# Performance work log

Hardware: AMD Instinct MI355X
Metric: run time of the kernel (lower is better)

## Reference

```python
import jax, jax.numpy as jnp
import numpy as np
import math

B, L, D, H, FACTOR = 4, 2048, 256, 8, 5
DH = D // H

def setup_inputs() -> dict:
    key = jax.random.key(0)
    ks = jax.random.split(key, 12)
    s = 1.0 / math.sqrt(D)
    return {
        "q": jax.random.normal(ks[0], (B, L, D), jnp.float32),
        "k": jax.random.normal(ks[1], (B, L, D), jnp.float32),
        "v": jax.random.normal(ks[2], (B, L, D), jnp.float32),
        "Wq": jax.random.normal(ks[3], (D, D), jnp.float32) * s,
        "bq": jax.random.normal(ks[4], (D,), jnp.float32) * s,
        "Wk": jax.random.normal(ks[5], (D, D), jnp.float32) * s,
        "bk": jax.random.normal(ks[6], (D,), jnp.float32) * s,
        "Wv": jax.random.normal(ks[7], (D, D), jnp.float32) * s,
        "bv": jax.random.normal(ks[8], (D,), jnp.float32) * s,
        "Wc": jax.random.normal(ks[9], (D, D), jnp.float32) * s,
        "bc": jax.random.normal(ks[10], (D,), jnp.float32) * s,
        "index_sample": jax.random.randint(ks[11], (L,), 0, L),  # U_part = min(5*L*ceil(log1p(L)), L) = L
    }

def reference(q, k, v, Wq, bq, Wk, bk, Wv, bv, Wc, bc, index_sample):
    # projections (torch Linear: x @ W^T + b)
    qp = q @ Wq.T + bq
    kp = k @ Wk.T + bk
    vp = v @ Wv.T + bv
    # NOTE: original reshapes q with a raw view (no transpose), k/v via split()
    q4 = qp.reshape(B, H, L, DH)                       # faithful to q.view(B, H, L, dh)
    k4 = kp.reshape(B, L, H, DH).transpose(0, 2, 1, 3)
    v4 = vp.reshape(B, L, H, DH).transpose(0, 2, 1, 3)
    qf = q4.reshape(B * H, L, DH)
    kf = k4.reshape(B * H, L, DH)
    vf = v4.reshape(B * H, L, DH)
    # random K sampling (with replacement); U_part == L here
    K_sample = kf[:, index_sample, :]                  # [BH, L, dh]
    QK = jnp.einsum('bld,bud->blu', qf, K_sample)      # [BH, L, L]
    M = QK.max(axis=-1) - QK.sum(axis=-1) / L          # sparsity measure [BH, L]
    u = min(FACTOR * math.ceil(math.log1p(L)), L)      # = 40
    _, top_idx = jax.lax.top_k(-M, u)                  # topk(..., largest=False)
    Q_red = jnp.take_along_axis(qf, top_idx[:, :, None], axis=1)  # [BH, u, dh]
    scores = jnp.einsum('bud,bld->bul', Q_red, kf) / math.sqrt(DH)
    probs = jax.nn.softmax(scores, axis=-1)
    out = jnp.einsum('bul,bld->bud', probs, vf)        # [BH, u, dh]
    out = out.reshape(B, H, u, DH).transpose(0, 2, 1, 3).reshape(B, u, D)
    return out @ Wc.T + bc
```

## Files before the change

### kernel.cpp

```cpp
#include <hip/hip_runtime.h>
#include <math.h>

#define B_ 4
#define L_ 2048
#define D_ 256
#define H_ 8
#define DH_ 32
#define NH_ 32
#define U_ 40
#define LD_ 524288
#define NCH_ 16

typedef __attribute__((ext_vector_type(8))) short short8;
typedef __attribute__((ext_vector_type(4))) float floatx4;

static __device__ __forceinline__ unsigned long long ullmin_(unsigned long long a, unsigned long long b) {
    return a < b ? a : b;
}
static __device__ __forceinline__ unsigned short f2bf_rne(float x) {
    unsigned u = __float_as_uint(x);
    unsigned r = u + 0x7FFFu + ((u >> 16) & 1u);
    return (unsigned short)(r >> 16);
}
static __device__ __forceinline__ float bf2f(unsigned short h) {
    return __uint_as_float(((unsigned)h) << 16);
}

__global__ __launch_bounds__(256) void gemm_mfma3(const float* __restrict__ q,
                                                  const float* __restrict__ k,
                                                  const float* __restrict__ v,
                                                  const float* __restrict__ Wq,
                                                  const float* __restrict__ Wk,
                                                  const float* __restrict__ Wv,
                                                  const float* __restrict__ bq,
                                                  const float* __restrict__ bk,
                                                  const float* __restrict__ bv,
                                                  float* __restrict__ qp,
                                                  float* __restrict__ kp,
                                                  float* __restrict__ vp) {
    const int mat = blockIdx.z;
    const float* X = (mat == 0) ? q : (mat == 1) ? k : v;
    const float* W = (mat == 0) ? Wq : (mat == 1) ? Wk : Wv;
    const float* bias = (mat == 0) ? bq : (mat == 1) ? bk : bv;
    float* Y = (mat == 0) ? qp : (mat == 1) ? kp : vp;

    const int t = threadIdx.x;
    const int w = t >> 6, lane = t & 63;
    const int lq = lane & 15, quad = lane >> 4;
    const int colBase = blockIdx.y * 64;
    const int rowBaseW = blockIdx.x * 128 + w * 32;

    __shared__ unsigned short Bls[24576];

    floatx4 acc[2][4];
#pragma unroll
    for (int mt = 0; mt < 2; ++mt)
#pragma unroll
        for (int nt = 0; nt < 4; ++nt) acc[mt][nt] = (floatx4){0.f, 0.f, 0.f, 0.f};

    for (int phase = 0; phase < 2; ++phase) {
        __syncthreads();
#pragma unroll
        for (int r = 0; r < 8; ++r) {
            const int e = t + 256 * r;
            const int col = e >> 5;
            const int k4u = e & 31;
            const int kk = phase * 128 + k4u * 4;
            const float4 x = *(const float4*)(W + (size_t)(colBase + col) * 256 + kk);
            float xs[4] = {x.x, x.y, x.z, x.w};
            unsigned short hv[4], mv4[4], lv[4];
#pragma unroll
            for (int j = 0; j < 4; ++j) {
                hv[j] = f2bf_rne(xs[j]);
                const float e1 = xs[j] - bf2f(hv[j]);
                mv4[j] = f2bf_rne(e1);
                const float e2 = e1 - bf2f(mv4[j]);
                lv[j] = f2bf_rne(e2);
            }
            const int nt = col >> 4, cin = col & 15;
            const int ktl = k4u >> 3, kin = (k4u & 7) * 4;
            const int base = nt * 512 + cin * 32 + kin;
            *(ushort4*)&Bls[((0 * 4 + ktl) << 11) + base] = make_ushort4(hv[0], hv[1], hv[2], hv[3]);
            *(ushort4*)&Bls[((1 * 4 + ktl) << 11) + base] = make_ushort4(mv4[0], mv4[1], mv4[2], mv4[3]);
            *(ushort4*)&Bls[((2 * 4 + ktl) << 11) + base] = make_ushort4(lv[0], lv[1], lv[2], lv[3]);
        }
        __syncthreads();

#pragma unroll
        for (int ktl = 0; ktl < 4; ++ktl) {
            const int kt = phase * 4 + ktl;
            short8 Bh[4], Bm[4], Bl[4];
            const int fo = lq * 32 + quad * 8;
#pragma unroll
            for (int j = 0; j < 4; ++j) {
                Bh[j] = *(const short8*)&Bls[((0 * 4 + ktl) << 11) + j * 512 + fo];
                Bm[j] = *(const short8*)&Bls[((1 * 4 + ktl) << 11) + j * 512 + fo];
                Bl[j] = *(const short8*)&Bls[((2 * 4 + ktl) << 11) + j * 512 + fo];
            }
#pragma unroll
            for (int mt = 0; mt < 2; ++mt) {
                const int m = rowBaseW + mt * 16 + lq;
                short8 Ah, Am, Al;
                {
                    const float* xr = X + (size_t)m * 256 + kt * 32 + quad * 8;
                    const float4 x0 = *(const float4*)xr;
                    const float4 x1 = *(const float4*)(xr + 4);
                    float xs[8] = {x0.x, x0.y, x0.z, x0.w, x1.x, x1.y, x1.z, x1.w};
#pragma unroll
                    for (int j = 0; j < 8; ++j) {
                        const unsigned short h = f2bf_rne(xs[j]);
                        const float e1 = xs[j] - bf2f(h);
                        const unsigned short md = f2bf_rne(e1);
                        const float e2 = e1 - bf2f(md);
                        Ah[j] = (short)h;
                        Am[j] = (short)md;
                        Al[j] = (short)f2bf_rne(e2);
                    }
                }
#pragma unroll
                for (int j = 0; j < 4; ++j) {
                    floatx4 a = acc[mt][j];
                    a = __builtin_amdgcn_mfma_f32_16x16x32_bf16(Am, Bm[j], a, 0, 0, 0);
                    a = __builtin_amdgcn_mfma_f32_16x16x32_bf16(Ah, Bl[j], a, 0, 0, 0);
                    a = __builtin_amdgcn_mfma_f32_16x16x32_bf16(Al, Bh[j], a, 0, 0, 0);
                    a = __builtin_amdgcn_mfma_f32_16x16x32_bf16(Ah, Bm[j], a, 0, 0, 0);
                    a = __builtin_amdgcn_mfma_f32_16x16x32_bf16(Am, Bh[j], a, 0, 0, 0);
                    a = __builtin_amdgcn_mfma_f32_16x16x32_bf16(Ah, Bh[j], a, 0, 0, 0);
                    acc[mt][j] = a;
                }
            }
        }
    }

#pragma unroll
    for (int mt = 0; mt < 2; ++mt)
#pragma unroll
        for (int nt = 0; nt < 4; ++nt) {
            const int c = colBase + nt * 16 + lq;
            const float bv_ = bias[c];
#pragma unroll
            for (int r = 0; r < 4; ++r) {
                const int mr = rowBaseW + mt * 16 + quad * 4 + r;
                Y[(size_t)mr * 256 + c] = acc[mt][nt][r] + bv_;
            }
        }
}

__global__ __launch_bounds__(64) void gemm_out(const float* __restrict__ X,
                                               const float* __restrict__ Wc,
                                               const float* __restrict__ bias,
                                               float* __restrict__ Y) {
    const int lane = threadIdx.x;
    const int lq = lane & 15, quad = lane >> 4;
    const int rowBase = blockIdx.x * 16;
    const int colBase = blockIdx.y * 64;

    floatx4 acc[4];
#pragma unroll
    for (int nt = 0; nt < 4; ++nt) acc[nt] = (floatx4){0.f, 0.f, 0.f, 0.f};

#pragma unroll
    for (int kt = 0; kt < 8; ++kt) {
        short8 Ah, Am, Al;
        {
            const float* xr = X + (size_t)(rowBase + lq) * 256 + kt * 32 + quad * 8;
            const float4 x0 = *(const float4*)xr;
            const float4 x1 = *(const float4*)(xr + 4);
            float xs[8] = {x0.x, x0.y, x0.z, x0.w, x1.x, x1.y, x1.z, x1.w};
#pragma unroll
            for (int j = 0; j < 8; ++j) {
                const unsigned short h = f2bf_rne(xs[j]);
                const float e1 = xs[j] - bf2f(h);
                const unsigned short md = f2bf_rne(e1);
                const float e2 = e1 - bf2f(md);
                Ah[j] = (short)h;
                Am[j] = (short)md;
                Al[j] = (short)f2bf_rne(e2);
            }
        }
        short8 Bh[4], Bm[4], Bl[4];
#pragma unroll
        for (int nt = 0; nt < 4; ++nt) {
            const float* wr = Wc + (size_t)(colBase + nt * 16 + lq) * 256 + kt * 32 + quad * 8;
            const float4 x0 = *(const float4*)wr;
            const float4 x1 = *(const float4*)(wr + 4);
            float xs[8] = {x0.x, x0.y, x0.z, x0.w, x1.x, x1.y, x1.z, x1.w};
#pragma unroll
            for (int j = 0; j < 8; ++j) {
                const unsigned short h = f2bf_rne(xs[j]);
                const float e1 = xs[j] - bf2f(h);
                const unsigned short md = f2bf_rne(e1);
                const float e2 = e1 - bf2f(md);
                Bh[nt][j] = (short)h;
                Bm[nt][j] = (short)md;
                Bl[nt][j] = (short)f2bf_rne(e2);
            }
        }
#pragma unroll
        for (int nt = 0; nt < 4; ++nt) {
            floatx4 a = acc[nt];
            a = __builtin_amdgcn_mfma_f32_16x16x32_bf16(Am, Bm[nt], a, 0, 0, 0);
            a = __builtin_amdgcn_mfma_f32_16x16x32_bf16(Ah, Bl[nt], a, 0, 0, 0);
            a = __builtin_amdgcn_mfma_f32_16x16x32_bf16(Al, Bh[nt], a, 0, 0, 0);
            a = __builtin_amdgcn_mfma_f32_16x16x32_bf16(Ah, Bm[nt], a, 0, 0, 0);
            a = __builtin_amdgcn_mfma_f32_16x16x32_bf16(Am, Bh[nt], a, 0, 0, 0);
            a = __builtin_amdgcn_mfma_f32_16x16x32_bf16(Ah, Bh[nt], a, 0, 0, 0);
            acc[nt] = a;
        }
    }

#pragma unroll
    for (int nt = 0; nt < 4; ++nt) {
        const int c = colBase + nt * 16 + lq;
        const float bv = bias[c];
#pragma unroll
        for (int r = 0; r < 4; ++r) {
            const int mr = rowBase + quad * 4 + r;
            Y[(size_t)mr * 256 + c] = acc[nt][r] + bv;
        }
    }
}

__global__ __launch_bounds__(256) void kconv_ksum(const float* __restrict__ kp,
                                                  const int* __restrict__ idx,
                                                  unsigned short* __restrict__ Khi,
                                                  unsigned short* __restrict__ Klo,
                                                  float* __restrict__ Ksum32) {
    const int blk = blockIdx.x;
    const int i = blk >> 5, uc = blk & 31;
    const int b = i >> 3, h = i & 7;
    const int t = threadIdx.x;
    const int dq = (t & 7) * 4;
    const int ur = t >> 3;

    __shared__ float part[32][36];
    float ksum[4] = {0.f, 0.f, 0.f, 0.f};

#pragma unroll
    for (int p = 0; p < 2; ++p) {
        int u = uc * 64 + p * 32 + ur;
        const float4 x = *(const float4*)(kp + (size_t)b * LD_ + (size_t)idx[u] * D_ + h * DH_ + dq);
        float xs[4] = {x.x, x.y, x.z, x.w};
        unsigned short hv[4], lv[4];
#pragma unroll
        for (int j = 0; j < 4; ++j) {
            ksum[j] += xs[j];
            hv[j] = f2bf_rne(xs[j]);
            lv[j] = f2bf_rne(xs[j] - bf2f(hv[j]));
        }
        size_t o = ((size_t)i * 2048 + u) * 32 + dq;
        *(ushort4*)(Khi + o) = make_ushort4(hv[0], hv[1], hv[2], hv[3]);
        *(ushort4*)(Klo + o) = make_ushort4(lv[0], lv[1], lv[2], lv[3]);
    }
#pragma unroll
    for (int j = 0; j < 4; ++j) part[ur][dq + j] = ksum[j];
    __syncthreads();
    if (t < 32) {
        float s = 0.f;
#pragma unroll 8
        for (int u2 = 0; u2 < 32; ++u2) s += part[u2][t];
        Ksum32[(size_t)blk * 32 + t] = s;
    }
}

__global__ __launch_bounds__(256) void mpart_mfma(const float* __restrict__ qp,
                                                  const unsigned short* __restrict__ Khi,
                                                  const unsigned short* __restrict__ Klo,
                                                  const float* __restrict__ Ksum32,
                                                  float* __restrict__ Mv,
                                                  float* __restrict__ Qmean) {
    const int blk = blockIdx.x;
    const int i = blk >> 5;
    const int lg = blk & 31;
    const int t = threadIdx.x;
    const int w = t >> 6;
    const int lane = t & 63;
    const int lq = lane & 15;
    const int quad = lane >> 4;

    __shared__ float ssum[32];
    __shared__ float red[4][64];
    if (t < 32) {
        float s = 0.f;
#pragma unroll 8
        for (int uc = 0; uc < 32; ++uc) s += Ksum32[((size_t)i * 32 + uc) * 32 + t];
        ssum[t] = s;
    }

    short8 Ah[4], Al[4];
#pragma unroll
    for (int lt = 0; lt < 4; ++lt) {
        const int l = lg * 64 + lt * 16 + lq;
        const float* qrow = qp + ((size_t)i * 2048 + l) * 32 + quad * 8;
        float4 x0 = *(const float4*)(qrow);
        float4 x1 = *(const float4*)(qrow + 4);
        float xs[8] = {x0.x, x0.y, x0.z, x0.w, x1.x, x1.y, x1.z, x1.w};
#pragma unroll
        for (int j = 0; j < 8; ++j) {
            unsigned short h = f2bf_rne(xs[j]);
            unsigned short lo = f2bf_rne(xs[j] - bf2f(h));
            Ah[lt][j] = (short)h;
            Al[lt][j] = (short)lo;
        }
    }

    floatx4 rmax[4];
#pragma unroll
    for (int lt = 0; lt < 4; ++lt)
        rmax[lt] = (floatx4){-INFINITY, -INFINITY, -INFINITY, -INFINITY};

    const size_t kfrag = ((size_t)i * 2048 + w * 512 + lq) * 32 + quad * 8;
    const unsigned short* ph = Khi + kfrag;
    const unsigned short* pl = Klo + kfrag;
#pragma unroll 2
    for (int s = 0; s < 32; ++s) {
        short8 Bh = *(const short8*)(ph + (size_t)s * 512);
        short8 Bl = *(const short8*)(pl + (size_t)s * 512);
#pragma unroll
        for (int lt = 0; lt < 4; ++lt) {
            floatx4 acc = (floatx4){0.f, 0.f, 0.f, 0.f};
            acc = __builtin_amdgcn_mfma_f32_16x16x32_bf16(Al[lt], Bh, acc, 0, 0, 0);
            acc = __builtin_amdgcn_mfma_f32_16x16x32_bf16(Ah[lt], Bl, acc, 0, 0, 0);
            acc = __builtin_amdgcn_mfma_f32_16x16x32_bf16(Ah[lt], Bh, acc, 0, 0, 0);
#pragma unroll
            for (int r = 0; r < 4; ++r) rmax[lt][r] = fmaxf(rmax[lt][r], acc[r]);
        }
    }

#pragma unroll
    for (int lt = 0; lt < 4; ++lt)
#pragma unroll
        for (int r = 0; r < 4; ++r) {
            float v = rmax[lt][r];
#pragma unroll
            for (int off = 1; off < 16; off <<= 1)
                v = fmaxf(v, __shfl_xor(v, off, 64));
            rmax[lt][r] = v;
        }
    if (lq == 0) {
#pragma unroll
        for (int lt = 0; lt < 4; ++lt)
#pragma unroll
            for (int r = 0; r < 4; ++r)
                red[w][lt * 16 + quad * 4 + r] = rmax[lt][r];
    }
    __syncthreads();
    if (t < 64) {
        const int l = lg * 64 + t;
        float m = fmaxf(fmaxf(red[0][t], red[1][t]), fmaxf(red[2][t], red[3][t]));
        const float4* q4 = (const float4*)(qp + ((size_t)i * 2048 + l) * 32);
        const float4* s4 = (const float4*)ssum;
        float qs = 0.f;
#pragma unroll
        for (int z = 0; z < 8; ++z) {
            float4 a = q4[z];
            float4 c = s4[z];
            qs = fmaf(a.x, c.x, qs);
            qs = fmaf(a.y, c.y, qs);
            qs = fmaf(a.z, c.z, qs);
            qs = fmaf(a.w, c.w, qs);
        }
        const float qm = qs * (1.0f / 2048.0f);
        Qmean[(size_t)i * 2048 + l] = qm;
        Mv[(size_t)i * 2048 + l] = m - qm;
    }
}

__global__ __launch_bounds__(256) void topk64_kernel(const float* __restrict__ Mv,
                                                     int* __restrict__ candIdx) {
    const int i = blockIdx.x;
    const int t = threadIdx.x;
    unsigned long long keys[8];
    __shared__ unsigned long long wred[4];
#pragma unroll
    for (int j = 0; j < 8; ++j) {
        const int l = t + 256 * j;
        unsigned u32 = __float_as_uint(Mv[(size_t)i * 2048 + l]);
        u32 = (u32 & 0x80000000u) ? ~u32 : (u32 | 0x80000000u);
        keys[j] = ((unsigned long long)u32 << 32) | (unsigned)l;
    }
    for (int it = 0; it < 64; ++it) {
        unsigned long long best = keys[0];
#pragma unroll
        for (int j = 1; j < 8; ++j) best = ullmin_(best, keys[j]);
#pragma unroll
        for (int off = 1; off < 64; off <<= 1)
            best = ullmin_(best, __shfl_xor(best, off, 64));
        if ((t & 63) == 0) wred[t >> 6] = best;
        __syncthreads();
        const unsigned long long m = ullmin_(ullmin_(wred[0], wred[1]), ullmin_(wred[2], wred[3]));
        if (t == 0) candIdx[i * 64 + it] = (int)(m & 0xffffffffu);
#pragma unroll
        for (int j = 0; j < 8; ++j)
            if (keys[j] == m) keys[j] = ~0ULL;
        __syncthreads();
    }
}

__global__ __launch_bounds__(256) void refine_kernel(const float* __restrict__ qp,
                                                     const float* __restrict__ kp,
                                                     const int* __restrict__ idx,
                                                     const int* __restrict__ candIdx,
                                                     float* __restrict__ refPart) {
    const int blk = blockIdx.x;
    const int i = blk >> 3, c = blk & 7;
    const int b = i >> 3, h = i & 7;
    const int t = threadIdx.x;
    __shared__ float qc[64][40];
    __shared__ float Ks[128][40];

    {
        const int cand = t >> 2, dp = (t & 3) * 8;
        const int l = candIdx[i * 64 + cand];
        const float* src = qp + ((size_t)i * 2048 + l) * 32 + dp;
        *(float4*)&qc[cand][dp] = *(const float4*)(src);
        *(float4*)&qc[cand][dp + 4] = *(const float4*)(src + 4);
    }
    __syncthreads();

    const int cand = t >> 2, usub = t & 3;
    float qv[32];
#pragma unroll
    for (int z = 0; z < 8; ++z) {
        float4 a = *(const float4*)&qc[cand][z * 4];
        qv[4 * z] = a.x; qv[4 * z + 1] = a.y; qv[4 * z + 2] = a.z; qv[4 * z + 3] = a.w;
    }

    float m = -INFINITY;
    for (int s = 0; s < 2; ++s) {
        {
            const int r = t >> 1, half = t & 1;
            const int u = c * 256 + s * 128 + r;
            const float* krow = kp + (size_t)b * LD_ + (size_t)idx[u] * D_ + h * DH_ + half * 16;
#pragma unroll
            for (int z = 0; z < 4; ++z)
                *(float4*)&Ks[r][half * 16 + z * 4] = *(const float4*)(krow + z * 4);
        }
        __syncthreads();
        for (int ur = usub; ur < 128; ur += 4) {
            float a0 = 0, a1 = 0, a2 = 0, a3 = 0;
#pragma unroll
            for (int z = 0; z < 8; ++z) {
                float4 kv = *(const float4*)&Ks[ur][z * 4];
                a0 = fmaf(qv[4 * z], kv.x, a0);
                a1 = fmaf(qv[4 * z + 1], kv.y, a1);
                a2 = fmaf(qv[4 * z + 2], kv.z, a2);
                a3 = fmaf(qv[4 * z + 3], kv.w, a3);
            }
            m = fmaxf(m, (a0 + a1) + (a2 + a3));
        }
        __syncthreads();
    }
    m = fmaxf(m, __shfl_xor(m, 1, 64));
    m = fmaxf(m, __shfl_xor(m, 2, 64));
    if ((t & 3) == 0) refPart[((size_t)i * 8 + c) * 64 + cand] = m;
}

__global__ __launch_bounds__(64) void select40_kernel(const int* __restrict__ candIdx,
                                                      const float* __restrict__ refPart,
                                                      const float* __restrict__ Qmean,
                                                      int* __restrict__ topIdx) {
    const int i = blockIdx.x;
    const int t = threadIdx.x;
    const int l = candIdx[i * 64 + t];
    float m = -INFINITY;
#pragma unroll
    for (int c = 0; c < 8; ++c) m = fmaxf(m, refPart[((size_t)i * 8 + c) * 64 + t]);
    float Mex = m - Qmean[(size_t)i * 2048 + l];
    unsigned u32 = __float_as_uint(Mex);
    u32 = (u32 & 0x80000000u) ? ~u32 : (u32 | 0x80000000u);
    unsigned long long key = ((unsigned long long)u32 << 32) | (unsigned)l;
    for (int it = 0; it < 40; ++it) {
        unsigned long long k2 = key;
#pragma unroll
        for (int off = 1; off < 64; off <<= 1) k2 = ullmin_(k2, __shfl_xor(k2, off, 64));
        if (key == k2) {
            topIdx[i * 40 + it] = l;
            key = ~0ULL;
        }
    }
}

#define SCP2 136
#define VSP 36

__global__ __launch_bounds__(320) void attn_part(const float* __restrict__ qp,
                                                 const float* __restrict__ kp,
                                                 const float* __restrict__ vp,
                                                 const int* __restrict__ topIdx,
                                                 float* __restrict__ mPart,
                                                 float* __restrict__ sPart,
                                                 float* __restrict__ oPart) {
    const int blk = blockIdx.x;
    const int i = blk >> 4, c = blk & 15;
    const int b = i >> 3, h = i & 7;
    const int t = threadIdx.x;

    __shared__ float Qs[40][32];
    __shared__ float Vs[128][VSP];
    __shared__ float sc[40][SCP2];
    __shared__ float mred[40], sred[40];

    {
        const int r = t >> 3, qq = t & 7;
        const int lq = topIdx[i * 40 + r];
        *(float4*)&Qs[r][qq * 4] = *(const float4*)(qp + ((size_t)i * 2048 + lq) * 32 + qq * 4);
    }
    for (int e = t; e < 1024; e += 320) {
        const int r = e >> 3, qq = e & 7;
        *(float4*)&Vs[r][qq * 4] =
            *(const float4*)(vp + (size_t)b * LD_ + (size_t)(c * 128 + r) * 256 + h * 32 + qq * 4);
    }
    __syncthreads();

    const float scale = 0.17677669529663687f;

    if (t < 256) {
        const int r = t >> 1;
        const int j0 = (t & 1) * 20;
        const float* kr = kp + (size_t)b * LD_ + (size_t)(c * 128 + r) * 256 + h * 32;
        float kv[32];
#pragma unroll
        for (int z = 0; z < 8; ++z) {
            float4 x = *(const float4*)(kr + z * 4);
            kv[4 * z] = x.x; kv[4 * z + 1] = x.y; kv[4 * z + 2] = x.z; kv[4 * z + 3] = x.w;
        }
#pragma unroll 4
        for (int jj = 0; jj < 20; ++jj) {
            const int j = j0 + jj;
            float a0 = 0, a1 = 0, a2 = 0, a3 = 0;
#pragma unroll
            for (int z = 0; z < 8; ++z) {
                const float4 q4 = *(const float4*)&Qs[j][z * 4];
                a0 = fmaf(kv[4 * z], q4.x, a0);
                a1 = fmaf(kv[4 * z + 1], q4.y, a1);
                a2 = fmaf(kv[4 * z + 2], q4.z, a2);
                a3 = fmaf(kv[4 * z + 3], q4.w, a3);
            }
            sc[j][r] = ((a0 + a1) + (a2 + a3)) * scale;
        }
    }
    __syncthreads();

    {
        const int w = t >> 6, lane = t & 63;
#pragma unroll
        for (int rr = 0; rr < 8; ++rr) {
            const int j = w * 8 + rr;
            float x0 = sc[j][lane], x1 = sc[j][lane + 64];
            float m = fmaxf(x0, x1);
#pragma unroll
            for (int off = 1; off < 64; off <<= 1) m = fmaxf(m, __shfl_xor(m, off, 64));
            const float e0 = __expf(x0 - m), e1 = __expf(x1 - m);
            sc[j][lane] = e0; sc[j][lane + 64] = e1;
            float s = e0 + e1;
#pragma unroll
            for (int off = 1; off < 64; off <<= 1) s += __shfl_xor(s, off, 64);
            if (lane == 0) { mred[j] = m; sred[j] = s; }
        }
    }
    __syncthreads();

    {
        const int j = t >> 3, qq = t & 7;
        float4 acc = make_float4(0.f, 0.f, 0.f, 0.f);
        for (int l = 0; l < 128; ++l) {
            const float p = sc[j][l];
            const float4 v4 = *(const float4*)&Vs[l][qq * 4];
            acc.x = fmaf(p, v4.x, acc.x);
            acc.y = fmaf(p, v4.y, acc.y);
            acc.z = fmaf(p, v4.z, acc.z);
            acc.w = fmaf(p, v4.w, acc.w);
        }
        const size_t o = (size_t)(i * NCH_ + c) * 40 + j;
        *(float4*)&oPart[o * 32 + qq * 4] = acc;
        if (qq == 0) { mPart[o] = mred[j]; sPart[o] = sred[j]; }
    }
}

__global__ __launch_bounds__(256) void attn_combine(const float* __restrict__ mPart,
                                                    const float* __restrict__ sPart,
                                                    const float* __restrict__ oPart,
                                                    float* __restrict__ attnOut) {
    const int i = blockIdx.x;
    const int b = i >> 3, h = i & 7;
    const int t = threadIdx.x;
    for (int e = t; e < 1280; e += 256) {
        const int j = e >> 5, d = e & 31;
        float mv[NCH_];
        float M = -INFINITY;
#pragma unroll
        for (int c = 0; c < NCH_; ++c) {
            mv[c] = mPart[(size_t)(i * NCH_ + c) * 40 + j];
            M = fmaxf(M, mv[c]);
        }
        float S = 0.f, O = 0.f;
#pragma unroll
        for (int c = 0; c < NCH_; ++c) {
            const float sc_ = __expf(mv[c] - M);
            const size_t o = (size_t)(i * NCH_ + c) * 40 + j;
            S = fmaf(sPart[o], sc_, S);
            O = fmaf(oPart[o * 32 + d], sc_, O);
        }
        attnOut[((size_t)b * 40 + j) * 256 + h * 32 + d] = O / S;
    }
}

extern "C" void kernel_launch(void* const* d_in, const int* in_sizes, int n_in,
                              void* d_out, int out_size, void* d_ws, size_t ws_size,
                              hipStream_t stream) {
    const float* q  = (const float*)d_in[0];
    const float* k  = (const float*)d_in[1];
    const float* v  = (const float*)d_in[2];
    const float* Wq = (const float*)d_in[3];
    const float* bq = (const float*)d_in[4];
    const float* Wk = (const float*)d_in[5];
    const float* bk = (const float*)d_in[6];
    const float* Wv = (const float*)d_in[7];
    const float* bv = (const float*)d_in[8];
    const float* Wc = (const float*)d_in[9];
    const float* bc = (const float*)d_in[10];
    const int* idx  = (const int*)d_in[11];
    float* out = (float*)d_out;

    char* w = (char*)d_ws;
    float*          qp      = (float*)(w);
    float*          kp      = (float*)(w + (8u << 20));
    float*          vp      = (float*)(w + (16u << 20));
    unsigned short* Khi     = (unsigned short*)(w + (24u << 20));
    unsigned short* Klo     = (unsigned short*)(w + (28u << 20));
    float*          Mv      = (float*)(w + (32u << 20));
    float*          Qmean   = (float*)(w + (32u << 20) + (256u << 10));
    float*          Ksum32  = (float*)(w + (32u << 20) + (512u << 10));
    int*            candIdx = (int*)  (w + (32u << 20) + (640u << 10));
    int*            topIdx  = (int*)  (w + (32u << 20) + (648u << 10));
    float*          refPart = (float*)(w + (32u << 20) + (656u << 10));
    float*          attnOut = (float*)(w + (32u << 20) + (720u << 10));
    float*          mPart   = (float*)(w + (24u << 20));
    float*          sPart   = (float*)(w + (24u << 20) + (128u << 10));
    float*          oPart   = (float*)(w + (24u << 20) + (256u << 10));

    hipLaunchKernelGGL(gemm_mfma3, dim3(64, 4, 3), dim3(256), 0, stream,
                       q, k, v, Wq, Wk, Wv, bq, bk, bv, qp, kp, vp);
    hipLaunchKernelGGL(kconv_ksum, dim3(1024), dim3(256), 0, stream, kp, idx, Khi, Klo, Ksum32);
    hipLaunchKernelGGL(mpart_mfma, dim3(1024), dim3(256), 0, stream, qp, Khi, Klo, Ksum32, Mv, Qmean);
    hipLaunchKernelGGL(topk64_kernel, dim3(32), dim3(256), 0, stream, Mv, candIdx);
    hipLaunchKernelGGL(refine_kernel, dim3(256), dim3(256), 0, stream, qp, kp, idx, candIdx, refPart);
    hipLaunchKernelGGL(select40_kernel, dim3(32), dim3(64), 0, stream, candIdx, refPart, Qmean, topIdx);
    hipLaunchKernelGGL(attn_part, dim3(512), dim3(320), 0, stream, qp, kp, vp, topIdx, mPart, sPart, oPart);
    hipLaunchKernelGGL(attn_combine, dim3(32), dim3(256), 0, stream, mPart, sPart, oPart, attnOut);
    hipLaunchKernelGGL(gemm_out, dim3(10, 4), dim3(64), 0, stream, attnOut, Wc, bc, out);
}
```

Baseline: 246.9 us.

## Fuse top-64 candidate selection into refine and top-40 selection into attention

Drops the separate topk64 and select40 kernels. Each refine block now redundantly computes the top-64 candidates from Mv (8x redundant per head), and each attention block redundantly recomputes the final top-40 from the refine partials (16x redundant per head). This removes two launches and their serial gaps on tiny grids, at the cost of duplicated selection work and an extra barrier in each block.

```diff
diff --git a/kernel.cpp b/kernel.cpp
--- a/kernel.cpp
+++ b/kernel.cpp
@@ -366,52 +366,52 @@
     }
 }
 
-__global__ __launch_bounds__(256) void topk64_kernel(const float* __restrict__ Mv,
-                                                     int* __restrict__ candIdx) {
-    const int i = blockIdx.x;
-    const int t = threadIdx.x;
-    unsigned long long keys[8];
-    __shared__ unsigned long long wred[4];
-#pragma unroll
-    for (int j = 0; j < 8; ++j) {
-        const int l = t + 256 * j;
-        unsigned u32 = __float_as_uint(Mv[(size_t)i * 2048 + l]);
-        u32 = (u32 & 0x80000000u) ? ~u32 : (u32 | 0x80000000u);
-        keys[j] = ((unsigned long long)u32 << 32) | (unsigned)l;
-    }
-    for (int it = 0; it < 64; ++it) {
-        unsigned long long best = keys[0];
-#pragma unroll
-        for (int j = 1; j < 8; ++j) best = ullmin_(best, keys[j]);
-#pragma unroll
-        for (int off = 1; off < 64; off <<= 1)
-            best = ullmin_(best, __shfl_xor(best, off, 64));
-        if ((t & 63) == 0) wred[t >> 6] = best;
-        __syncthreads();
-        const unsigned long long m = ullmin_(ullmin_(wred[0], wred[1]), ullmin_(wred[2], wred[3]));
-        if (t == 0) candIdx[i * 64 + it] = (int)(m & 0xffffffffu);
-#pragma unroll
-        for (int j = 0; j < 8; ++j)
-            if (keys[j] == m) keys[j] = ~0ULL;
-        __syncthreads();
-    }
-}
-
-__global__ __launch_bounds__(256) void refine_kernel(const float* __restrict__ qp,
+__global__ __launch_bounds__(256) void refine_kernel(const float* __restrict__ Mv,
+                                                     const float* __restrict__ qp,
                                                      const float* __restrict__ kp,
                                                      const int* __restrict__ idx,
-                                                     const int* __restrict__ candIdx,
+                                                     int* __restrict__ candIdx,
                                                      float* __restrict__ refPart) {
     const int blk = blockIdx.x;
     const int i = blk >> 3, c = blk & 7;
     const int b = i >> 3, h = i & 7;
     const int t = threadIdx.x;
+    __shared__ unsigned long long wred[4];
+    __shared__ int candL[64];
     __shared__ float qc[64][40];
     __shared__ float Ks[128][40];
 
     {
+        unsigned long long keys[8];
+#pragma unroll
+        for (int j = 0; j < 8; ++j) {
+            const int l = t + 256 * j;
+            unsigned u32 = __float_as_uint(Mv[(size_t)i * 2048 + l]);
+            u32 = (u32 & 0x80000000u) ? ~u32 : (u32 | 0x80000000u);
+            keys[j] = ((unsigned long long)u32 << 32) | (unsigned)l;
+        }
+        for (int it = 0; it < 64; ++it) {
+            unsigned long long best = keys[0];
+#pragma unroll
+            for (int j = 1; j < 8; ++j) best = ullmin_(best, keys[j]);
+#pragma unroll
+            for (int off = 1; off < 64; off <<= 1)
+                best = ullmin_(best, __shfl_xor(best, off, 64));
+            if ((t & 63) == 0) wred[t >> 6] = best;
+            __syncthreads();
+            const unsigned long long m = ullmin_(ullmin_(wred[0], wred[1]), ullmin_(wred[2], wred[3]));
+            if (t == 0) candL[it] = (int)(m & 0xffffffffu);
+#pragma unroll
+            for (int j = 0; j < 8; ++j)
+                if (keys[j] == m) keys[j] = ~0ULL;
+            __syncthreads();
+        }
+    }
+    if (c == 0 && t < 64) candIdx[i * 64 + t] = candL[t];
+
+    {
         const int cand = t >> 2, dp = (t & 3) * 8;
-        const int l = candIdx[i * 64 + cand];
+        const int l = candL[cand];
         const float* src = qp + ((size_t)i * 2048 + l) * 32 + dp;
         *(float4*)&qc[cand][dp] = *(const float4*)(src);
         *(float4*)&qc[cand][dp + 4] = *(const float4*)(src + 4);
@@ -456,38 +456,15 @@
     if ((t & 3) == 0) refPart[((size_t)i * 8 + c) * 64 + cand] = m;
 }
 
-__global__ __launch_bounds__(64) void select40_kernel(const int* __restrict__ candIdx,
-                                                      const float* __restrict__ refPart,
-                                                      const float* __restrict__ Qmean,
-                                                      int* __restrict__ topIdx) {
-    const int i = blockIdx.x;
-    const int t = threadIdx.x;
-    const int l = candIdx[i * 64 + t];
-    float m = -INFINITY;
-#pragma unroll
-    for (int c = 0; c < 8; ++c) m = fmaxf(m, refPart[((size_t)i * 8 + c) * 64 + t]);
-    float Mex = m - Qmean[(size_t)i * 2048 + l];
-    unsigned u32 = __float_as_uint(Mex);
-    u32 = (u32 & 0x80000000u) ? ~u32 : (u32 | 0x80000000u);
-    unsigned long long key = ((unsigned long long)u32 << 32) | (unsigned)l;
-    for (int it = 0; it < 40; ++it) {
-        unsigned long long k2 = key;
-#pragma unroll
-        for (int off = 1; off < 64; off <<= 1) k2 = ullmin_(k2, __shfl_xor(k2, off, 64));
-        if (key == k2) {
-            topIdx[i * 40 + it] = l;
-            key = ~0ULL;
-        }
-    }
-}
-
 #define SCP2 136
 #define VSP 36
 
 __global__ __launch_bounds__(320) void attn_part(const float* __restrict__ qp,
                                                  const float* __restrict__ kp,
                                                  const float* __restrict__ vp,
-                                                 const int* __restrict__ topIdx,
+                                                 const int* __restrict__ candIdx,
+                                                 const float* __restrict__ refPart,
+                                                 const float* __restrict__ Qmean,
                                                  float* __restrict__ mPart,
                                                  float* __restrict__ sPart,
                                                  float* __restrict__ oPart) {
@@ -496,20 +473,42 @@
     const int b = i >> 3, h = i & 7;
     const int t = threadIdx.x;
 
+    __shared__ int topL[40];
     __shared__ float Qs[40][32];
     __shared__ float Vs[128][VSP];
     __shared__ float sc[40][SCP2];
     __shared__ float mred[40], sred[40];
 
-    {
-        const int r = t >> 3, qq = t & 7;
-        const int lq = topIdx[i * 40 + r];
-        *(float4*)&Qs[r][qq * 4] = *(const float4*)(qp + ((size_t)i * 2048 + lq) * 32 + qq * 4);
+    if (t < 64) {
+        const int l = candIdx[i * 64 + t];
+        float m = -INFINITY;
+#pragma unroll
+        for (int cc = 0; cc < 8; ++cc) m = fmaxf(m, refPart[((size_t)i * 8 + cc) * 64 + t]);
+        const float Mex = m - Qmean[(size_t)i * 2048 + l];
+        unsigned u32 = __float_as_uint(Mex);
+        u32 = (u32 & 0x80000000u) ? ~u32 : (u32 | 0x80000000u);
+        unsigned long long key = ((unsigned long long)u32 << 32) | (unsigned)l;
+        for (int it = 0; it < 40; ++it) {
+            unsigned long long k2 = key;
+#pragma unroll
+            for (int off = 1; off < 64; off <<= 1) k2 = ullmin_(k2, __shfl_xor(k2, off, 64));
+            if (key == k2) {
+                topL[it] = l;
+                key = ~0ULL;
+            }
+        }
     }
     for (int e = t; e < 1024; e += 320) {
         const int r = e >> 3, qq = e & 7;
         *(float4*)&Vs[r][qq * 4] =
             *(const float4*)(vp + (size_t)b * LD_ + (size_t)(c * 128 + r) * 256 + h * 32 + qq * 4);
+    }
+    __syncthreads();
+
+    {
+        const int r = t >> 3, qq = t & 7;
+        const int lq = topL[r];
+        *(float4*)&Qs[r][qq * 4] = *(const float4*)(qp + ((size_t)i * 2048 + lq) * 32 + qq * 4);
     }
     __syncthreads();
 
@@ -633,7 +632,6 @@
     float*          Qmean   = (float*)(w + (32u << 20) + (256u << 10));
     float*          Ksum32  = (float*)(w + (32u << 20) + (512u << 10));
     int*            candIdx = (int*)  (w + (32u << 20) + (640u << 10));
-    int*            topIdx  = (int*)  (w + (32u << 20) + (648u << 10));
     float*          refPart = (float*)(w + (32u << 20) + (656u << 10));
     float*          attnOut = (float*)(w + (32u << 20) + (720u << 10));
     float*          mPart   = (float*)(w + (24u << 20));
@@ -644,10 +642,9 @@
                        q, k, v, Wq, Wk, Wv, bq, bk, bv, qp, kp, vp);
     hipLaunchKernelGGL(kconv_ksum, dim3(1024), dim3(256), 0, stream, kp, idx, Khi, Klo, Ksum32);
     hipLaunchKernelGGL(mpart_mfma, dim3(1024), dim3(256), 0, stream, qp, Khi, Klo, Ksum32, Mv, Qmean);
-    hipLaunchKernelGGL(topk64_kernel, dim3(32), dim3(256), 0, stream, Mv, candIdx);
-    hipLaunchKernelGGL(refine_kernel, dim3(256), dim3(256), 0, stream, qp, kp, idx, candIdx, refPart);
-    hipLaunchKernelGGL(select40_kernel, dim3(32), dim3(64), 0, stream, candIdx, refPart, Qmean, topIdx);
-    hipLaunchKernelGGL(attn_part, dim3(512), dim3(320), 0, stream, qp, kp, vp, topIdx, mPart, sPart, oPart);
+    hipLaunchKernelGGL(refine_kernel, dim3(256), dim3(256), 0, stream, Mv, qp, kp, idx, candIdx, refPart);
+    hipLaunchKernelGGL(attn_part, dim3(512), dim3(320), 0, stream, qp, kp, vp, candIdx, refPart, Qmean,
+                       mPart, sPart, oPart);
     hipLaunchKernelGGL(attn_combine, dim3(32), dim3(256), 0, stream, mPart, sPart, oPart, attnOut);
     hipLaunchKernelGGL(gemm_out, dim3(10, 4), dim3(64), 0, stream, attnOut, Wc, bc, out);
 }
```

Result: no change. 247.4 us (+0.2%).
